# Kernel optimization log

Measured on AMD Instinct MI355X. Metric: run time of the kernel, lower is better.

Reference implementation:

```python
import jax, jax.numpy as jnp
import numpy as np

N_HEAD = 16
D_MODEL = 2048
ROPE_BASE = 10000.0


def setup_inputs() -> dict:
    key = jax.random.key(0)
    k1, k2, k3 = jax.random.split(key, 3)
    b, s, d = 2, 2048, D_MODEL
    x = jax.random.normal(k1, (b, s, d), dtype=jnp.float32)
    # torch nn.Linear init scale ~ 1/sqrt(fan_in); keep activations sane
    W_qkv = jax.random.normal(k2, (3 * d, d), dtype=jnp.float32) * (d ** -0.5)
    W_o = jax.random.normal(k3, (d, d), dtype=jnp.float32) * (d ** -0.5)
    return {"x": x, "W_qkv": W_qkv, "W_o": W_o}


def _rotate_half(x):
    x1, x2 = jnp.split(x, 2, axis=-1)
    return jnp.concatenate((-x2, x1), axis=-1)


def _rope_cos_sin(seq_len, d_head, dtype):
    inv_freq = 1.0 / (ROPE_BASE ** (jnp.arange(0, d_head, 2, dtype=jnp.float32) / d_head))
    t = jnp.arange(seq_len, dtype=jnp.float32)
    freqs = jnp.einsum("i,j->ij", t, inv_freq)          # [s, d_head/2]
    emb = jnp.concatenate((freqs, freqs), axis=-1)       # [s, d_head]
    return jnp.cos(emb).astype(dtype)[None, None], jnp.sin(emb).astype(dtype)[None, None]


def reference(x, W_qkv, W_o):
    b, s, d = x.shape
    h = N_HEAD
    dh = d // h
    qkv = x @ W_qkv.T                                    # [b, s, 3d]
    qkv = qkv.reshape(b, s, 3, h, dh)
    q, k, v = (jnp.transpose(qkv[:, :, i], (0, 2, 1, 3)) for i in range(3))  # [b, h, s, dh]
    cos, sin = _rope_cos_sin(s, dh, x.dtype)
    q = q * cos + _rotate_half(q) * sin
    k = k * cos + _rotate_half(k) * sin
    scale = dh ** -0.5
    scores = jnp.einsum("bhqd,bhkd->bhqk", q, k) * scale  # [b, h, s, s]
    causal = jnp.tril(jnp.ones((s, s), dtype=bool))
    scores = jnp.where(causal[None, None], scores, jnp.finfo(scores.dtype).min)
    attn = jax.nn.softmax(scores, axis=-1)
    z = jnp.einsum("bhqk,bhkd->bhqd", attn, v)            # [b, h, s, dh]
    z = jnp.transpose(z, (0, 2, 1, 3)).reshape(b, s, d)
    return z @ W_o.T
```

## Files before the change

### kernel.cpp

```cpp
#include <hip/hip_runtime.h>
#include <stdint.h>
#include <stddef.h>

typedef __attribute__((ext_vector_type(8))) short bf16x8;
typedef __attribute__((ext_vector_type(4))) float f32x4;
typedef __attribute__((ext_vector_type(16))) float f32x16;
typedef __attribute__((ext_vector_type(4))) unsigned int u32x4;

#define AS1 __attribute__((address_space(1)))
#define AS3 __attribute__((address_space(3)))

__device__ __forceinline__ void gll16(const void* g, void* l) {
  __builtin_amdgcn_global_load_lds((const AS1 unsigned int*)g, (AS3 unsigned int*)l, 16, 0, 0);
}

__device__ __forceinline__ uint16_t f2bf(float f) {
  uint32_t u = __builtin_bit_cast(uint32_t, f);
  u += 0x7fffu + ((u >> 16) & 1u);
  return (uint16_t)(u >> 16);
}
__device__ __forceinline__ float bf2f(uint16_t h) {
  uint32_t u = ((uint32_t)h) << 16;
  return __builtin_bit_cast(float, u);
}
__device__ __forceinline__ uint32_t pack2bf(float lo, float hi) {
  return (uint32_t)f2bf(lo) | ((uint32_t)f2bf(hi) << 16);
}

#define BARRIER() do { asm volatile("" ::: "memory"); __builtin_amdgcn_s_barrier(); asm volatile("" ::: "memory"); } while (0)

__global__ void cvt_f32_bf16(const float* __restrict__ in, uint16_t* __restrict__ out, int n8) {
  int i = blockIdx.x * blockDim.x + threadIdx.x;
  if (i >= n8) return;
  float4 a = reinterpret_cast<const float4*>(in)[2 * i];
  float4 b = reinterpret_cast<const float4*>(in)[2 * i + 1];
  union { uint16_t h[8]; u32x4 v; } u;
  u.h[0] = f2bf(a.x); u.h[1] = f2bf(a.y); u.h[2] = f2bf(a.z); u.h[3] = f2bf(a.w);
  u.h[4] = f2bf(b.x); u.h[5] = f2bf(b.y); u.h[6] = f2bf(b.z); u.h[7] = f2bf(b.w);
  reinterpret_cast<u32x4*>(out)[i] = u.v;
}

__global__ void rope_table(float* __restrict__ cosT, float* __restrict__ sinT) {
  int idx = blockIdx.x * blockDim.x + threadIdx.x;
  int s = idx >> 6, i = idx & 63;
  float invf = expf(-(float)i * (9.2103403719761836f / 64.0f));
  float f = (float)s * invf;
  cosT[idx] = cosf(f);
  sinT[idx] = sinf(f);
}

__global__ void rope_apply2(uint16_t* __restrict__ Qb, uint16_t* __restrict__ Kb,
                            const float* __restrict__ cosT, const float* __restrict__ sinT) {
  int idx = blockIdx.x * blockDim.x + threadIdx.x;
  uint16_t* buf = (idx < 4194304) ? Qb : Kb;
  int id = idx & 4194303;
  int i = id & 63;
  int s = (id >> 6) & 2047;
  int bh = id >> 17;
  size_t base = ((size_t)bh * 2048 + s) * 128;
  float x0 = bf2f(buf[base + i]);
  float x1 = bf2f(buf[base + i + 64]);
  float c = cosT[(s << 6) + i], sn = sinT[(s << 6) + i];
  buf[base + i]      = f2bf(x0 * c - x1 * sn);
  buf[base + i + 64] = f2bf(x1 * c + x0 * sn);
}

__global__ __launch_bounds__(512, 2) void gemm_qkv(
    const uint16_t* __restrict__ A,
    const uint16_t* __restrict__ B,
    uint16_t* __restrict__ Qb, uint16_t* __restrict__ Kb, uint16_t* __restrict__ Vt) {
  extern __shared__ uint16_t L[];
  const int t = threadIdx.x, lane = t & 63, w = t >> 6;
  const int fr = lane & 15, fg = lane >> 4;
  const int wm = w >> 2, wn = w & 3;
  const int flat = blockIdx.y * 16 + blockIdx.x;
  const int swz = (flat & 7) * 48 + (flat >> 3);
  const int m0 = (swz & 15) * 256, n0 = (swz >> 4) * 256;

  f32x4 acc[8][4];
#pragma unroll
  for (int i = 0; i < 8; i++)
#pragma unroll
    for (int j = 0; j < 4; j++) acc[i][j] = (f32x4)(0.0f);

#define ST(kt, ab, half)                                                          \
  do {                                                                            \
    if ((kt) < 32) {                                                              \
      const uint16_t* src_ = (ab) ? B : A;                                        \
      int g0_ = ((ab) ? n0 : m0) + (half) * 128;                                  \
      uint16_t* dst_ = &L[((((kt) & 1) * 2 + (ab)) * 2 + (half)) * 8192];         \
      _Pragma("unroll")                                                           \
      for (int j_ = 0; j_ < 2; ++j_) {                                            \
        int c_ = t + j_ * 512;                                                    \
        int row_ = c_ >> 3, cc_ = c_ & 7, scc_ = cc_ ^ (row_ & 7);                \
        gll16(&src_[(size_t)(g0_ + row_) * 2048 + (kt) * 64 + scc_ * 8],          \
              &dst_[(c_ & ~63) * 8]);                                             \
      }                                                                           \
    }                                                                             \
  } while (0)

  auto LDA4 = [&](bf16x8 (&af)[8], int buf, int mh) {
#pragma unroll
    for (int mi = 0; mi < 4; ++mi)
#pragma unroll
      for (int ks = 0; ks < 2; ++ks) {
        int lr = (mh * 4 + mi) * 16 + fr;
        int ck = (ks * 4 + fg) ^ (lr & 7);
        af[mi * 2 + ks] = *(const bf16x8*)&L[((buf * 2 + 0) * 2 + wm) * 8192 + lr * 64 + ck * 8];
      }
  };
  auto LDB2 = [&](bf16x8 (&bfr)[4], int buf, int nh) {
#pragma unroll
    for (int ni = 0; ni < 2; ++ni)
#pragma unroll
      for (int ks = 0; ks < 2; ++ks) {
        int rn = (wn & 1) * 64 + (nh * 2 + ni) * 16 + fr;
        int ck = (ks * 4 + fg) ^ (rn & 7);
        bfr[ni * 2 + ks] = *(const bf16x8*)&L[((buf * 2 + 1) * 2 + (wn >> 1)) * 8192 + rn * 64 + ck * 8];
      }
  };
  auto MF16 = [&](bf16x8 (&af)[8], bf16x8 (&bfr)[4], int mh, int nh) {
    __builtin_amdgcn_s_setprio(1);
#pragma unroll
    for (int mi = 0; mi < 4; ++mi)
#pragma unroll
      for (int ni = 0; ni < 2; ++ni)
#pragma unroll
        for (int ks = 0; ks < 2; ++ks)
          acc[mh * 4 + mi][nh * 2 + ni] = __builtin_amdgcn_mfma_f32_16x16x32_bf16(
              af[mi * 2 + ks], bfr[ni * 2 + ks], acc[mh * 4 + mi][nh * 2 + ni], 0, 0, 0);
    __builtin_amdgcn_s_setprio(0);
  };

  ST(0, 0, 0); ST(0, 0, 1); ST(0, 1, 0); ST(0, 1, 1); ST(1, 0, 0);
  asm volatile("s_waitcnt vmcnt(2)" ::: "memory");
  BARRIER();

  for (int tl = 0; tl < 32; ++tl) {
    const int buf = tl & 1;
    bf16x8 af[8], bA[4], bB[4];
    LDA4(af, buf, 0); LDB2(bA, buf, 0); ST(tl + 1, 0, 1);
    BARRIER(); MF16(af, bA, 0, 0); BARRIER();
    LDB2(bB, buf, 1); ST(tl + 1, 1, 0);
    BARRIER(); MF16(af, bB, 0, 1); BARRIER();
    LDA4(af, buf, 1); ST(tl + 1, 1, 1);
    BARRIER(); MF16(af, bA, 1, 0); BARRIER();
    ST(tl + 2, 0, 0);
    BARRIER(); MF16(af, bB, 1, 1);
    if (tl < 30) asm volatile("s_waitcnt vmcnt(2)" ::: "memory");
    else         asm volatile("s_waitcnt vmcnt(0)" ::: "memory");
    BARRIER();
  }
#undef ST

#pragma unroll
  for (int mi = 0; mi < 8; ++mi) {
#pragma unroll
    for (int ni = 0; ni < 4; ++ni) {
      int ng = n0 + wn * 64 + ni * 16 + fr;
      int head = (ng >> 7) & 15, dd = ng & 127;
      if (ng < 4096) {
        uint16_t* dst = (ng < 2048) ? Qb : Kb;
#pragma unroll
        for (int r = 0; r < 4; r++) {
          int mg = m0 + wm * 128 + mi * 16 + fg * 4 + r;
          int b = mg >> 11, si = mg & 2047;
          dst[((size_t)(b * 16 + head) * 2048 + si) * 128 + dd] = f2bf(acc[mi][ni][r]);
        }
      } else {
        uint2 pv = make_uint2(pack2bf(acc[mi][ni][0], acc[mi][ni][1]),
                              pack2bf(acc[mi][ni][2], acc[mi][ni][3]));
        int mg = m0 + wm * 128 + mi * 16 + fg * 4;
        int b = mg >> 11, si = mg & 2047;
        *(uint2*)&Vt[((size_t)(b * 16 + head) * 128 + dd) * 2048 + si] = pv;
      }
    }
  }
}

__global__ __launch_bounds__(256) void gemm_out_k(
    const uint16_t* __restrict__ A,
    const uint16_t* __restrict__ B,
    float* __restrict__ C) {
  __shared__ uint16_t Ash[3][128 * 32];
  __shared__ uint16_t Bsh[3][128 * 32];
  const int t = threadIdx.x;
  const int lane = t & 63;
  const int w = t >> 6, wr = w >> 1, wc = w & 1;
  const int fr = lane & 15, fg = lane >> 4, fk = fg * 8;
  const int m0 = blockIdx.x * 128, n0 = blockIdx.y * 128;
  const int K = 2048;
  const int T = K / 32;
  const int c0 = t, c1 = t + 256;

  f32x4 acc[4][4];
#pragma unroll
  for (int i = 0; i < 4; i++)
#pragma unroll
    for (int j = 0; j < 4; j++) acc[i][j] = (f32x4)(0.0f);

#define OUT_STAGE(tile, buf)                                                        \
  {                                                                                 \
    int kt_ = (tile) * 32;                                                          \
    gll16(&A[(size_t)(m0 + (c0 >> 2)) * K + kt_ + (c0 & 3) * 8], &Ash[buf][(c0 & ~63) * 8]); \
    gll16(&A[(size_t)(m0 + (c1 >> 2)) * K + kt_ + (c1 & 3) * 8], &Ash[buf][(c1 & ~63) * 8]); \
    gll16(&B[(size_t)(n0 + (c0 >> 2)) * K + kt_ + (c0 & 3) * 8], &Bsh[buf][(c0 & ~63) * 8]); \
    gll16(&B[(size_t)(n0 + (c1 >> 2)) * K + kt_ + (c1 & 3) * 8], &Bsh[buf][(c1 & ~63) * 8]); \
  }

  OUT_STAGE(0, 0);
  OUT_STAGE(1, 1);
  asm volatile("s_waitcnt vmcnt(4)" ::: "memory");
  BARRIER();

  for (int tl = 0; tl < T; ++tl) {
    const int cur = tl % 3;
    if (tl + 2 < T) OUT_STAGE(tl + 2, (tl + 2) % 3);
    bf16x8 af[4], bfr[4];
#pragma unroll
    for (int mi = 0; mi < 4; mi++) af[mi] = *(const bf16x8*)&Ash[cur][(wr * 64 + mi * 16 + fr) * 32 + fk];
#pragma unroll
    for (int ni = 0; ni < 4; ni++) bfr[ni] = *(const bf16x8*)&Bsh[cur][(wc * 64 + ni * 16 + fr) * 32 + fk];
    __builtin_amdgcn_s_setprio(1);
#pragma unroll
    for (int mi = 0; mi < 4; mi++)
#pragma unroll
      for (int ni = 0; ni < 4; ni++)
        acc[mi][ni] = __builtin_amdgcn_mfma_f32_16x16x32_bf16(af[mi], bfr[ni], acc[mi][ni], 0, 0, 0);
    __builtin_amdgcn_s_setprio(0);
    if (tl + 2 < T) {
      asm volatile("s_waitcnt vmcnt(4)" ::: "memory");
    } else {
      asm volatile("s_waitcnt vmcnt(0)" ::: "memory");
    }
    BARRIER();
  }
#undef OUT_STAGE

#pragma unroll
  for (int mi = 0; mi < 4; mi++) {
#pragma unroll
    for (int ni = 0; ni < 4; ni++) {
      int ng = n0 + wc * 64 + ni * 16 + fr;
#pragma unroll
      for (int r = 0; r < 4; r++) {
        int mg = m0 + wr * 64 + mi * 16 + fg * 4 + r;
        C[(size_t)mg * 2048 + ng] = acc[mi][ni][r];
      }
    }
  }
}

__device__ __forceinline__ bf16x8 mk_pa(uint32_t p0, uint32_t p1, uint32_t p2, uint32_t p3, int hi) {
  uint32_t x0 = (uint32_t)__shfl_xor((int)p0, 32, 64);
  uint32_t x1 = (uint32_t)__shfl_xor((int)p1, 32, 64);
  uint32_t x2 = (uint32_t)__shfl_xor((int)p2, 32, 64);
  uint32_t x3 = (uint32_t)__shfl_xor((int)p3, 32, 64);
  u32x4 v;
  v[0] = hi ? x2 : p0;
  v[1] = hi ? x3 : p1;
  v[2] = hi ? p2 : x0;
  v[3] = hi ? p3 : x1;
  return __builtin_bit_cast(bf16x8, v);
}

__global__ __launch_bounds__(256, 2) void attn_kernel(
    const uint16_t* __restrict__ Qb, const uint16_t* __restrict__ Kb,
    const uint16_t* __restrict__ Vt, uint16_t* __restrict__ zb) {
  __shared__ uint16_t Ksh[2][64 * 128];
  __shared__ uint16_t Vsh[2][128 * 64];

  const int t = threadIdx.x, lane = t & 63, w = t >> 6;
  const int l31 = lane & 31, hi = lane >> 5;
  const int bx = blockIdx.x, bh = blockIdx.y;
  const int qt = (bh & 16) ? (15 - bx) : bx;
  const int q0 = qt * 128;
  const int qg = q0 + w * 32 + l31;
  const size_t hbase = (size_t)bh * 2048 * 128;
  const float scale2 = 0.08838834764831845f * 1.4426950408889634f;

#define ATT_STAGE(kt, buf)                                                        \
  do {                                                                            \
    const uint16_t* Kg_ = Kb + hbase + (size_t)(kt) * 64 * 128;                   \
    const uint16_t* Vg_ = Vt + hbase + (size_t)(kt) * 64;                         \
    _Pragma("unroll")                                                             \
    for (int i_ = 0; i_ < 4; i_++) {                                              \
      int c_ = t + i_ * 256;                                                      \
      { int row_ = c_ >> 4, cc_ = c_ & 15, scc_ = cc_ ^ (row_ & 7);               \
        gll16(&Kg_[row_ * 128 + scc_ * 8], &Ksh[buf][(c_ & ~63) * 8]); }          \
      { int r_ = c_ >> 3, cc_ = c_ & 7, scc_ = cc_ ^ (r_ & 7);                    \
        gll16(&Vg_[(size_t)r_ * 2048 + scc_ * 8], &Vsh[buf][(c_ & ~63) * 8]); }   \
    }                                                                             \
  } while (0)

  bf16x8 qf[8];
#pragma unroll
  for (int dc = 0; dc < 8; ++dc)
    qf[dc] = *(const bf16x8*)&Qb[hbase + (size_t)qg * 128 + dc * 16 + hi * 8];

  f32x16 oacc[4];
#pragma unroll
  for (int i = 0; i < 4; i++) oacc[i] = (f32x16)(0.0f);
  float mrow = -1e30f, lrow = 0.0f;

  const int ktiles = 2 * qt + 2;
  ATT_STAGE(0, 0);
  asm volatile("s_waitcnt vmcnt(0)" ::: "memory");
  BARRIER();

  for (int kt = 0; kt < ktiles; ++kt) {
    const int cur = kt & 1;
    if (kt + 1 < ktiles) ATT_STAGE(kt + 1, cur ^ 1);

    const int kv_base = kt * 64;
    if (kv_base <= q0 + w * 32 + 31) {
      f32x16 s0 = (f32x16)(0.0f), s1 = (f32x16)(0.0f);
      __builtin_amdgcn_s_setprio(1);
#pragma unroll
      for (int dc = 0; dc < 8; ++dc) {
        int ch = dc * 2 + hi;
        bf16x8 k0 = *(const bf16x8*)&Ksh[cur][l31 * 128 + ((ch ^ (l31 & 7)) * 8)];
        bf16x8 k1 = *(const bf16x8*)&Ksh[cur][(32 + l31) * 128 + ((ch ^ (l31 & 7)) * 8)];
        s0 = __builtin_amdgcn_mfma_f32_32x32x16_bf16(k0, qf[dc], s0, 0, 0, 0);
        s1 = __builtin_amdgcn_mfma_f32_32x32x16_bf16(k1, qf[dc], s1, 0, 0, 0);
      }
      __builtin_amdgcn_s_setprio(0);

      const bool need_mask = (kv_base + 63 > q0 + w * 32);
#pragma unroll
      for (int reg = 0; reg < 16; ++reg) {
        int koff = (reg & 3) + 8 * (reg >> 2) + 4 * hi;
        float a0 = s0[reg] * scale2, a1 = s1[reg] * scale2;
        if (need_mask) {
          if (kv_base + koff > qg) a0 = -1e30f;
          if (kv_base + 32 + koff > qg) a1 = -1e30f;
        }
        s0[reg] = a0; s1[reg] = a1;
      }

      float pmax = -1e30f;
#pragma unroll
      for (int reg = 0; reg < 16; ++reg) pmax = fmaxf(pmax, fmaxf(s0[reg], s1[reg]));
      pmax = fmaxf(pmax, __shfl_xor(pmax, 32, 64));

      bool defer = __all(pmax <= mrow + 8.0f);
      if (!defer) {
        float mnew = fmaxf(mrow, pmax);
        float al = exp2f(mrow - mnew);
        lrow *= al;
#pragma unroll
        for (int reg = 0; reg < 16; ++reg) {
          int src = (reg & 3) + 8 * (reg >> 2) + 4 * hi;
          float ar = __shfl(al, src, 64);
#pragma unroll
          for (int n = 0; n < 4; ++n) oacc[n][reg] *= ar;
        }
        mrow = mnew;
      }

      float ps = 0.0f;
      uint32_t pk0[8], pk1[8];
#pragma unroll
      for (int i = 0; i < 8; ++i) {
        float a = exp2f(s0[2 * i] - mrow), b = exp2f(s0[2 * i + 1] - mrow);
        ps += a + b;
        pk0[i] = pack2bf(a, b);
        float c = exp2f(s1[2 * i] - mrow), d = exp2f(s1[2 * i + 1] - mrow);
        ps += c + d;
        pk1[i] = pack2bf(c, d);
      }
      ps += __shfl_xor(ps, 32, 64);
      lrow += ps;

      bf16x8 pa[4];
      pa[0] = mk_pa(pk0[0], pk0[1], pk0[2], pk0[3], hi);
      pa[1] = mk_pa(pk0[4], pk0[5], pk0[6], pk0[7], hi);
      pa[2] = mk_pa(pk1[0], pk1[1], pk1[2], pk1[3], hi);
      pa[3] = mk_pa(pk1[4], pk1[5], pk1[6], pk1[7], hi);

      __builtin_amdgcn_s_setprio(1);
#pragma unroll
      for (int ksl = 0; ksl < 4; ++ksl) {
        int ch = ksl * 2 + hi;
#pragma unroll
        for (int n = 0; n < 4; ++n) {
          int d = n * 32 + l31;
          bf16x8 vf = *(const bf16x8*)&Vsh[cur][d * 64 + ((ch ^ (d & 7)) * 8)];
          oacc[n] = __builtin_amdgcn_mfma_f32_32x32x16_bf16(pa[ksl], vf, oacc[n], 0, 0, 0);
        }
      }
      __builtin_amdgcn_s_setprio(0);
    }

    asm volatile("s_waitcnt vmcnt(0)" ::: "memory");
    BARRIER();
  }
#undef ATT_STAGE

  const int b = bh >> 4, h = bh & 15;
#pragma unroll
  for (int reg = 0; reg < 16; ++reg) {
    int rloc = (reg & 3) + 8 * (reg >> 2) + 4 * hi;
    float linv = 1.0f / __shfl(lrow, rloc, 64);
    int rowg = q0 + w * 32 + rloc;
    size_t base = ((size_t)b * 2048 + rowg) * 2048 + h * 128 + l31;
#pragma unroll
    for (int n = 0; n < 4; ++n)
      zb[base + n * 32] = f2bf(oacc[n][reg] * linv);
  }
}

extern "C" void kernel_launch(void* const* d_in, const int* in_sizes, int n_in,
                              void* d_out, int out_size, void* d_ws, size_t ws_size,
                              hipStream_t stream) {
  const float* x    = (const float*)d_in[0];
  const float* Wqkv = (const float*)d_in[1];
  const float* Wo   = (const float*)d_in[2];
  float* out = (float*)d_out;
  char* ws = (char*)d_ws;

  uint16_t* Qb    = (uint16_t*)(ws + 0);
  uint16_t* Kb    = (uint16_t*)(ws + 16777216);
  uint16_t* Vt    = (uint16_t*)(ws + 33554432);
  uint16_t* xb    = (uint16_t*)(ws + 50331648);
  uint16_t* zb    = (uint16_t*)(ws + 50331648);
  uint16_t* wqkvb = (uint16_t*)(ws + 67108864);
  uint16_t* wob   = (uint16_t*)(ws + 92274688);
  float*    cosT  = (float*)   (ws + 100663296);
  float*    sinT  = (float*)   (ws + 101187584);

  cvt_f32_bf16<<<4096, 256, 0, stream>>>(x, xb, 8388608 / 8);
  cvt_f32_bf16<<<6144, 256, 0, stream>>>(Wqkv, wqkvb, 12582912 / 8);
  cvt_f32_bf16<<<2048, 256, 0, stream>>>(Wo, wob, 4194304 / 8);
  rope_table<<<512, 256, 0, stream>>>(cosT, sinT);

  gemm_qkv<<<dim3(16, 24), 512, 131072, stream>>>(xb, wqkvb, Qb, Kb, Vt);

  rope_apply2<<<32768, 256, 0, stream>>>(Qb, Kb, cosT, sinT);

  attn_kernel<<<dim3(16, 32), 256, 0, stream>>>(Qb, Kb, Vt, zb);

  gemm_out_k<<<dim3(32, 16), 256, 0, stream>>>(zb, wob, out);
}
```

Baseline: 306.8 us.

## Retile QKV GEMM to 256x192 tiles and fuse the three f32-to-bf16 conversion kernels

The QKV GEMM tile changes from 256x256 to 256x192, so the grid grows from 384 to 512 blocks and fills the 256 CUs more evenly. LDS drops to 112KB and the B loads and MFMA schedule are rebuilt for three N-subtiles per wave. Separately, the three f32-to-bf16 conversion launches are merged into one kernel to cut launch overhead. The smaller N tile lowers arithmetic intensity per block, and the reworked load and barrier schedule could expose more memory latency.

```diff
diff --git a/kernel.cpp b/kernel.cpp
--- a/kernel.cpp
+++ b/kernel.cpp
@@ -29,15 +29,21 @@
 
 #define BARRIER() do { asm volatile("" ::: "memory"); __builtin_amdgcn_s_barrier(); asm volatile("" ::: "memory"); } while (0)
 
-__global__ void cvt_f32_bf16(const float* __restrict__ in, uint16_t* __restrict__ out, int n8) {
+__global__ void cvt_all(const float* __restrict__ x, const float* __restrict__ wqkv,
+                        const float* __restrict__ wo,
+                        uint16_t* __restrict__ xb, uint16_t* __restrict__ wqkvb,
+                        uint16_t* __restrict__ wob) {
   int i = blockIdx.x * blockDim.x + threadIdx.x;
-  if (i >= n8) return;
-  float4 a = reinterpret_cast<const float4*>(in)[2 * i];
-  float4 b = reinterpret_cast<const float4*>(in)[2 * i + 1];
+  const float* in; uint16_t* out; int off;
+  if (i < 1048576)      { in = x;    out = xb;    off = i; }
+  else if (i < 2621440) { in = wqkv; out = wqkvb; off = i - 1048576; }
+  else                  { in = wo;   out = wob;   off = i - 2621440; }
+  float4 a = reinterpret_cast<const float4*>(in)[2 * off];
+  float4 b = reinterpret_cast<const float4*>(in)[2 * off + 1];
   union { uint16_t h[8]; u32x4 v; } u;
   u.h[0] = f2bf(a.x); u.h[1] = f2bf(a.y); u.h[2] = f2bf(a.z); u.h[3] = f2bf(a.w);
   u.h[4] = f2bf(b.x); u.h[5] = f2bf(b.y); u.h[6] = f2bf(b.z); u.h[7] = f2bf(b.w);
-  reinterpret_cast<u32x4*>(out)[i] = u.v;
+  reinterpret_cast<u32x4*>(out)[off] = u.v;
 }
 
 __global__ void rope_table(float* __restrict__ cosT, float* __restrict__ sinT) {
@@ -74,31 +80,44 @@
   const int fr = lane & 15, fg = lane >> 4;
   const int wm = w >> 2, wn = w & 3;
   const int flat = blockIdx.y * 16 + blockIdx.x;
-  const int swz = (flat & 7) * 48 + (flat >> 3);
-  const int m0 = (swz & 15) * 256, n0 = (swz >> 4) * 256;
-
-  f32x4 acc[8][4];
+  const int swz = (flat & 7) * 64 + (flat >> 3);
+  const int m0 = (swz & 15) * 256, n0 = (swz >> 4) * 192;
+
+  f32x4 acc[8][3];
 #pragma unroll
   for (int i = 0; i < 8; i++)
 #pragma unroll
-    for (int j = 0; j < 4; j++) acc[i][j] = (f32x4)(0.0f);
-
-#define ST(kt, ab, half)                                                          \
+    for (int j = 0; j < 3; j++) acc[i][j] = (f32x4)(0.0f);
+
+#define STA(kt, half)                                                             \
   do {                                                                            \
     if ((kt) < 32) {                                                              \
-      const uint16_t* src_ = (ab) ? B : A;                                        \
-      int g0_ = ((ab) ? n0 : m0) + (half) * 128;                                  \
-      uint16_t* dst_ = &L[((((kt) & 1) * 2 + (ab)) * 2 + (half)) * 8192];         \
+      int g0_ = m0 + (half) * 128;                                                \
+      uint16_t* dst_ = &L[((kt) & 1) * 28672 + (half) * 8192];                    \
       _Pragma("unroll")                                                           \
       for (int j_ = 0; j_ < 2; ++j_) {                                            \
         int c_ = t + j_ * 512;                                                    \
         int row_ = c_ >> 3, cc_ = c_ & 7, scc_ = cc_ ^ (row_ & 7);                \
-        gll16(&src_[(size_t)(g0_ + row_) * 2048 + (kt) * 64 + scc_ * 8],          \
+        gll16(&A[(size_t)(g0_ + row_) * 2048 + (kt) * 64 + scc_ * 8],             \
               &dst_[(c_ & ~63) * 8]);                                             \
       }                                                                           \
     }                                                                             \
   } while (0)
 
+#define STB(kt)                                                                   \
+  do {                                                                            \
+    if ((kt) < 32) {                                                              \
+      uint16_t* dst_ = &L[((kt) & 1) * 28672 + 16384];                            \
+      _Pragma("unroll")                                                           \
+      for (int j_ = 0; j_ < 3; ++j_) {                                            \
+        int c_ = t + j_ * 512;                                                    \
+        int row_ = c_ >> 3, cc_ = c_ & 7, scc_ = cc_ ^ (row_ & 7);                \
+        gll16(&B[(size_t)(n0 + row_) * 2048 + (kt) * 64 + scc_ * 8],              \
+              &dst_[(c_ & ~63) * 8]);                                             \
+      }                                                                           \
+    }                                                                             \
+  } while (0)
+
   auto LDA4 = [&](bf16x8 (&af)[8], int buf, int mh) {
 #pragma unroll
     for (int mi = 0; mi < 4; ++mi)
@@ -106,58 +125,63 @@
       for (int ks = 0; ks < 2; ++ks) {
         int lr = (mh * 4 + mi) * 16 + fr;
         int ck = (ks * 4 + fg) ^ (lr & 7);
-        af[mi * 2 + ks] = *(const bf16x8*)&L[((buf * 2 + 0) * 2 + wm) * 8192 + lr * 64 + ck * 8];
+        af[mi * 2 + ks] = *(const bf16x8*)&L[buf * 28672 + wm * 8192 + lr * 64 + ck * 8];
       }
   };
-  auto LDB2 = [&](bf16x8 (&bfr)[4], int buf, int nh) {
-#pragma unroll
-    for (int ni = 0; ni < 2; ++ni)
+  auto LDB = [&](bf16x8* bfr, int buf, int ni0, int nn) {
+#pragma unroll
+    for (int ni = 0; ni < 2; ++ni) {
+      if (ni >= nn) break;
 #pragma unroll
       for (int ks = 0; ks < 2; ++ks) {
-        int rn = (wn & 1) * 64 + (nh * 2 + ni) * 16 + fr;
+        int rn = wn * 48 + (ni0 + ni) * 16 + fr;
         int ck = (ks * 4 + fg) ^ (rn & 7);
-        bfr[ni * 2 + ks] = *(const bf16x8*)&L[((buf * 2 + 1) * 2 + (wn >> 1)) * 8192 + rn * 64 + ck * 8];
-      }
+        bfr[ni * 2 + ks] = *(const bf16x8*)&L[buf * 28672 + 16384 + rn * 64 + ck * 8];
+      }
+    }
   };
-  auto MF16 = [&](bf16x8 (&af)[8], bf16x8 (&bfr)[4], int mh, int nh) {
+  auto MF = [&](bf16x8 (&af)[8], bf16x8* bfr, int mh, int ni0, int nn) {
     __builtin_amdgcn_s_setprio(1);
 #pragma unroll
     for (int mi = 0; mi < 4; ++mi)
 #pragma unroll
-      for (int ni = 0; ni < 2; ++ni)
+      for (int ni = 0; ni < 2; ++ni) {
+        if (ni >= nn) break;
 #pragma unroll
         for (int ks = 0; ks < 2; ++ks)
-          acc[mh * 4 + mi][nh * 2 + ni] = __builtin_amdgcn_mfma_f32_16x16x32_bf16(
-              af[mi * 2 + ks], bfr[ni * 2 + ks], acc[mh * 4 + mi][nh * 2 + ni], 0, 0, 0);
+          acc[mh * 4 + mi][ni0 + ni] = __builtin_amdgcn_mfma_f32_16x16x32_bf16(
+              af[mi * 2 + ks], bfr[ni * 2 + ks], acc[mh * 4 + mi][ni0 + ni], 0, 0, 0);
+      }
     __builtin_amdgcn_s_setprio(0);
   };
 
-  ST(0, 0, 0); ST(0, 0, 1); ST(0, 1, 0); ST(0, 1, 1); ST(1, 0, 0);
+  STA(0, 0); STA(0, 1); STB(0); STA(1, 0);
   asm volatile("s_waitcnt vmcnt(2)" ::: "memory");
   BARRIER();
 
   for (int tl = 0; tl < 32; ++tl) {
     const int buf = tl & 1;
     bf16x8 af[8], bA[4], bB[4];
-    LDA4(af, buf, 0); LDB2(bA, buf, 0); ST(tl + 1, 0, 1);
-    BARRIER(); MF16(af, bA, 0, 0); BARRIER();
-    LDB2(bB, buf, 1); ST(tl + 1, 1, 0);
-    BARRIER(); MF16(af, bB, 0, 1); BARRIER();
-    LDA4(af, buf, 1); ST(tl + 1, 1, 1);
-    BARRIER(); MF16(af, bA, 1, 0); BARRIER();
-    ST(tl + 2, 0, 0);
-    BARRIER(); MF16(af, bB, 1, 1);
+    LDA4(af, buf, 0); LDB(bA, buf, 0, 2); STA(tl + 1, 1);
+    BARRIER(); MF(af, bA, 0, 0, 2); BARRIER();
+    LDB(bB, buf, 2, 1); STB(tl + 1);
+    BARRIER(); MF(af, bB, 0, 2, 1); BARRIER();
+    LDA4(af, buf, 1);
+    BARRIER(); MF(af, bA, 1, 0, 2); BARRIER();
+    STA(tl + 2, 0);
+    BARRIER(); MF(af, bB, 1, 2, 1);
     if (tl < 30) asm volatile("s_waitcnt vmcnt(2)" ::: "memory");
     else         asm volatile("s_waitcnt vmcnt(0)" ::: "memory");
     BARRIER();
   }
-#undef ST
+#undef STA
+#undef STB
 
 #pragma unroll
   for (int mi = 0; mi < 8; ++mi) {
 #pragma unroll
-    for (int ni = 0; ni < 4; ++ni) {
-      int ng = n0 + wn * 64 + ni * 16 + fr;
+    for (int ni = 0; ni < 3; ++ni) {
+      int ng = n0 + wn * 48 + ni * 16 + fr;
       int head = (ng >> 7) & 15, dd = ng & 127;
       if (ng < 4096) {
         uint16_t* dst = (ng < 2048) ? Qb : Kb;
@@ -429,12 +453,10 @@
   float*    cosT  = (float*)   (ws + 100663296);
   float*    sinT  = (float*)   (ws + 101187584);
 
-  cvt_f32_bf16<<<4096, 256, 0, stream>>>(x, xb, 8388608 / 8);
-  cvt_f32_bf16<<<6144, 256, 0, stream>>>(Wqkv, wqkvb, 12582912 / 8);
-  cvt_f32_bf16<<<2048, 256, 0, stream>>>(Wo, wob, 4194304 / 8);
+  cvt_all<<<12288, 256, 0, stream>>>(x, Wqkv, Wo, xb, wqkvb, wob);
   rope_table<<<512, 256, 0, stream>>>(cosT, sinT);
 
-  gemm_qkv<<<dim3(16, 24), 512, 131072, stream>>>(xb, wqkvb, Qb, Kb, Vt);
+  gemm_qkv<<<dim3(16, 32), 512, 114688, stream>>>(xb, wqkvb, Qb, Kb, Vt);
 
   rope_apply2<<<32768, 256, 0, stream>>>(Qb, Kb, cosT, sinT);
 
```

New measurement: 294.0 us. 1.04x faster.
